# Performance work log

Measured on AMD Instinct MI355X. Metric: run time of the kernel, lower is better.

Reference implementation:

```python
import jax, jax.numpy as jnp
import numpy as np

N_NODES = 50000
N_EDGES = 800000
C_IN = 128
C_OUT = 256
BN_EPS = 1e-5


def setup_inputs() -> dict:
    key = jax.random.key(0)
    k1, k2, k3, k4, k5 = jax.random.split(key, 5)
    x = jax.random.normal(k1, (N_NODES, C_IN), dtype=jnp.float32)
    src = jax.random.randint(k2, (N_EDGES,), 0, N_NODES, dtype=jnp.int64)
    dst = jax.random.randint(k3, (N_EDGES,), 0, N_NODES, dtype=jnp.int64)
    theta_w = jax.random.normal(k4, (C_OUT, C_IN), dtype=jnp.float32) * 0.05
    phi_w = jax.random.normal(k5, (C_OUT, C_IN), dtype=jnp.float32) * 0.05
    gamma = jnp.ones((C_OUT,), dtype=jnp.float32)
    beta = jnp.zeros((C_OUT,), dtype=jnp.float32)
    return {"x": x, "src": src, "dst": dst, "theta_w": theta_w,
            "phi_w": phi_w, "gamma": gamma, "beta": beta}


def reference(x, src, dst, theta_w, phi_w, gamma, beta):
    # gather endpoint features: xi = x[src], xj = x[dst]
    xi = x[src]                      # [E, c_in]
    xj = x[dst]                      # [E, c_in]
    # e_ij = relu(theta(xj - xi) + phi(xi))  -> [E, c_out]
    e = jax.nn.relu((xj - xi) @ theta_w.T + xi @ phi_w.T)
    # scatter-max aggregate per source node; empty segments -> 0 (matches
    # torch.scatter_reduce amax with include_self=False leaving zeros)
    n = x.shape[0]
    agg = jax.ops.segment_max(e, src, num_segments=n)  # [N, c_out]
    agg = jnp.where(jnp.isneginf(agg), jnp.zeros((), agg.dtype), agg)
    # BatchNorm1d (training mode: batch statistics, biased variance)
    mean = jnp.mean(agg, axis=0)
    var = jnp.var(agg, axis=0)
    y = (agg - mean) * jax.lax.rsqrt(var + BN_EPS) * gamma + beta
    return jax.nn.relu(y)
```

## Files before the change

### kernel.cpp

```cpp
#include <hip/hip_runtime.h>

#define N_NODES 50000
#define N_EDGES 800000
#define C_IN 128
#define C_OUT 256
#define BN_EPS 1e-5f
#define NBLK ((N_NODES + 255) / 256)
#define SL 8
#define SLC 32
#define NPB 128
#define PAD 8
#define ECAP 3072

#define HB 782
#define GBX ((N_NODES + 127) / 128)
#define GB (GBX * 4)

using short8  = __attribute__((ext_vector_type(8))) short;
using floatx4 = __attribute__((ext_vector_type(4))) float;
using h2      = __attribute__((ext_vector_type(2))) _Float16;

union UH2 { unsigned int u; h2 h; };
union HS  { _Float16 f; unsigned short s; };

__device__ __forceinline__ h2 pkmax(h2 a, h2 b) {
    return __builtin_elementwise_max(a, b);
}

__device__ __forceinline__ unsigned short f2bf(float f) {
    unsigned int u = __float_as_uint(f);
    u = (u + 0x7fffu + ((u >> 16) & 1u)) >> 16;
    return (unsigned short)u;
}

#define XQ (N_NODES * C_IN / 4)
#define WQ (512 * C_IN / 4)

__global__ __launch_bounds__(256) void prep(
    const float* __restrict__ x, const float* __restrict__ theta,
    const float* __restrict__ phi, const int* __restrict__ src,
    unsigned short* __restrict__ xb, unsigned short* __restrict__ wb,
    int* __restrict__ deg, int* __restrict__ rank)
{
    const int tid = threadIdx.x;
    if (blockIdx.x < HB) {
        const int base = blockIdx.x * 1024 + tid;
        #pragma unroll
        for (int k = 0; k < 4; ++k) {
            int e = base + k * 256;
            if (e < N_EDGES) rank[e] = atomicAdd(&deg[src[e]], 1);
        }
        return;
    }
    int i = (blockIdx.x - HB) * 256 + tid;
    if (i < XQ) {
        float4 vv = ((const float4*)x)[i];
        ((ushort4*)xb)[i] = make_ushort4(f2bf(vv.x), f2bf(vv.y),
                                         f2bf(vv.z), f2bf(vv.w));
    } else if (i < XQ + WQ) {
        int j = i - XQ;
        float4 t;
        if (j < 256 * C_IN / 4) {
            t = ((const float4*)theta)[j];
        } else {
            int k = j - 256 * C_IN / 4;
            float4 th = ((const float4*)theta)[k];
            float4 ph = ((const float4*)phi)[k];
            t = make_float4(ph.x - th.x, ph.y - th.y, ph.z - th.z, ph.w - th.w);
        }
        ((ushort4*)wb)[j] = make_ushort4(f2bf(t.x), f2bf(t.y),
                                         f2bf(t.z), f2bf(t.w));
    }
}

__global__ __launch_bounds__(256) void scan_part(
    const int* __restrict__ deg, int* __restrict__ partials)
{
    __shared__ int s[256];
    const int tid = threadIdx.x;
    int i = blockIdx.x * 256 + tid;
    s[tid] = (i < N_NODES) ? deg[i] : 0;
    __syncthreads();
    for (int d = 128; d > 0; d >>= 1) {
        if (tid < d) s[tid] += s[tid + d];
        __syncthreads();
    }
    if (tid == 0) partials[blockIdx.x] = s[0];
}

__global__ __launch_bounds__(256) void scan_fin(
    const int* __restrict__ deg, const int* __restrict__ partials,
    int* __restrict__ off)
{
    __shared__ int s[256];
    const int tid = threadIdx.x;

    int pv = (tid < NBLK) ? partials[tid] : 0;
    s[tid] = pv;
    __syncthreads();
    for (int d = 1; d < 256; d <<= 1) {
        int t = (tid >= d) ? s[tid - d] : 0;
        __syncthreads();
        s[tid] += t;
        __syncthreads();
    }
    const int blockPrefix = (blockIdx.x == 0) ? 0 : s[blockIdx.x - 1];
    const int total = s[NBLK - 1];
    __syncthreads();

    int i = blockIdx.x * 256 + tid;
    int v = (i < N_NODES) ? deg[i] : 0;
    s[tid] = v;
    __syncthreads();
    for (int d = 1; d < 256; d <<= 1) {
        int t = (tid >= d) ? s[tid - d] : 0;
        __syncthreads();
        s[tid] += t;
        __syncthreads();
    }
    int ex = s[tid] - v + blockPrefix;
    if (i < N_NODES) off[i] = ex;
    if (blockIdx.x == 0 && tid == 0) off[N_NODES] = total;
}

__global__ __launch_bounds__(256) void gemm_scatter(
    const unsigned short* __restrict__ xb,
    const unsigned short* __restrict__ wb,
    unsigned short* __restrict__ u,
    unsigned short* __restrict__ v,
    const int* __restrict__ src, const int* __restrict__ dst,
    const int* __restrict__ off, const int* __restrict__ rank,
    int* __restrict__ edst)
{
    __shared__ unsigned short Bs[128][C_IN + PAD];
    const int tid = threadIdx.x;

    if (blockIdx.x < HB) {
        const int base = blockIdx.x * 1024 + tid;
        #pragma unroll
        for (int k = 0; k < 4; ++k) {
            int e = base + k * 256;
            if (e < N_EDGES) {
                int s = src[e];
                edst[off[s] + rank[e]] = dst[e];
            }
        }
        return;
    }

    const int b = blockIdx.x - HB;
    const int bx = b >> 2;
    const int by = b & 3;
    const int wave = tid >> 6;
    const int lane = tid & 63;
    const int l15 = lane & 15;
    const int quad = lane >> 4;

    {
        int r = tid >> 1;
        int cb = (tid & 1) * 64;
        const uint4* sp = (const uint4*)(wb + (size_t)(by * 128 + r) * C_IN + cb);
        #pragma unroll
        for (int i = 0; i < 8; ++i) *(uint4*)&Bs[r][cb + i * 8] = sp[i];
    }

    const int n0 = bx * 128 + wave * 32 + l15;
    const unsigned short* arow0 = xb + (size_t)min(n0,      N_NODES - 1) * C_IN + quad * 8;
    const unsigned short* arow1 = xb + (size_t)min(n0 + 16, N_NODES - 1) * C_IN + quad * 8;

    __syncthreads();

    floatx4 acc[2][8];
    #pragma unroll
    for (int mi = 0; mi < 2; ++mi)
        #pragma unroll
        for (int ni = 0; ni < 8; ++ni)
            acc[mi][ni] = (floatx4){0.f, 0.f, 0.f, 0.f};

    #pragma unroll
    for (int ks = 0; ks < 4; ++ks) {
        short8 a[2], bfr[8];
        a[0] = *(const short8*)(arow0 + ks * 32);
        a[1] = *(const short8*)(arow1 + ks * 32);
        #pragma unroll
        for (int ni = 0; ni < 8; ++ni)
            bfr[ni] = *(const short8*)&Bs[ni * 16 + l15][ks * 32 + quad * 8];
        #pragma unroll
        for (int mi = 0; mi < 2; ++mi)
            #pragma unroll
            for (int ni = 0; ni < 8; ++ni)
                acc[mi][ni] = __builtin_amdgcn_mfma_f32_16x16x32_bf16(
                    a[mi], bfr[ni], acc[mi][ni], 0, 0, 0);
    }

    const bool is_u = (by < 2);
    #pragma unroll
    for (int mi = 0; mi < 2; ++mi) {
        #pragma unroll
        for (int r = 0; r < 4; ++r) {
            int n = bx * 128 + wave * 32 + mi * 16 + quad * 4 + r;
            if (n >= N_NODES) continue;
            #pragma unroll
            for (int ni = 0; ni < 8; ++ni) {
                int c = by * 128 + ni * 16 + l15;
                HS hv; hv.f = (_Float16)acc[mi][ni][r];
                if (is_u) {
                    int s = c >> 5, o = c & 31;
                    u[((size_t)s * N_NODES + n) * SLC + o] = hv.s;
                } else {
                    int c2 = c - C_OUT;
                    int s = c2 >> 5, o = c2 & 31;
                    v[((size_t)s * N_NODES + n) * SLC + o] = hv.s;
                }
            }
        }
    }
}

__global__ __launch_bounds__(256) void gather_slice(
    const int* __restrict__ off, const int* __restrict__ edst,
    const unsigned short* __restrict__ u, const unsigned short* __restrict__ v,
    float* __restrict__ out, float* __restrict__ sums, float* __restrict__ sumsq)
{
    __shared__ int elds[ECAP];
    __shared__ int offs[NPB + 1];
    __shared__ float red[16][16][4];

    const int slice = blockIdx.x & 7;
    const int chunk = blockIdx.x >> 3;
    const int tid = threadIdx.x;
    const int g16 = tid >> 4;
    const int l16 = tid & 15;
    const int es  = l16 >> 2;
    const int c4  = l16 & 3;
    const int c16 = c4 * 16;
    const int cp  = c4 * 8 + es * 2;

    const int cn   = chunk * NPB;
    const int nend = min(cn + NPB, N_NODES);
    const int nloc = nend - cn;

    const int s0  = off[cn];
    const int cnt = off[nend] - s0;
    for (int t = tid; t <= nloc; t += 256) offs[t] = off[cn + t];
    const bool fits = (cnt <= ECAP);
    if (fits)
        for (int t = tid; t < cnt; t += 256) elds[t] = edst[s0 + t];
    __syncthreads();

    const char* ub = (const char*)(u + (size_t)slice * N_NODES * SLC);
    const unsigned short* vb = v + (size_t)slice * N_NODES * SLC;

    float s1_0 = 0.f, s1_1 = 0.f, s2_0 = 0.f, s2_1 = 0.f;

    auto gather_all = [&](auto fetch) {
        #pragma unroll 1
        for (int i = 0; i < NPB / 16; ++i) {
            const int nl = i * 16 + g16;
            const int n = cn + nl;
            if (n >= N_NODES) continue;
            const int start = offs[nl];
            const int end   = offs[nl + 1];

            UH2 m0, m1, m2, m3;
            m0.u = m1.u = m2.u = m3.u = 0xFC00FC00u;

            const int nit = (end - start + 15) >> 4;
            const int lim = end - 1;
            int b16 = start + es;
            for (int r = 0; r < nit; ++r, b16 += 16) {
                int i0 = min(b16,      lim);
                int i1 = min(b16 + 4,  lim);
                int i2 = min(b16 + 8,  lim);
                int i3 = min(b16 + 12, lim);
                int d0 = fetch(i0);
                int d1 = fetch(i1);
                int d2 = fetch(i2);
                int d3 = fetch(i3);
                uint4 w0 = *(const uint4*)(ub + ((d0 << 6) | c16));
                uint4 w1 = *(const uint4*)(ub + ((d1 << 6) | c16));
                uint4 w2 = *(const uint4*)(ub + ((d2 << 6) | c16));
                uint4 w3 = *(const uint4*)(ub + ((d3 << 6) | c16));
                UH2 a_, b_, c_, e_;
                a_.u = w0.x; b_.u = w1.x; c_.u = w2.x; e_.u = w3.x;
                m0.h = pkmax(m0.h, pkmax(pkmax(a_.h, b_.h), pkmax(c_.h, e_.h)));
                a_.u = w0.y; b_.u = w1.y; c_.u = w2.y; e_.u = w3.y;
                m1.h = pkmax(m1.h, pkmax(pkmax(a_.h, b_.h), pkmax(c_.h, e_.h)));
                a_.u = w0.z; b_.u = w1.z; c_.u = w2.z; e_.u = w3.z;
                m2.h = pkmax(m2.h, pkmax(pkmax(a_.h, b_.h), pkmax(c_.h, e_.h)));
                a_.u = w0.w; b_.u = w1.w; c_.u = w2.w; e_.u = w3.w;
                m3.h = pkmax(m3.h, pkmax(pkmax(a_.h, b_.h), pkmax(c_.h, e_.h)));
            }

            UH2 t;
            t.u = (unsigned)__shfl_xor((int)m0.u, 4); m0.h = pkmax(m0.h, t.h);
            t.u = (unsigned)__shfl_xor((int)m1.u, 4); m1.h = pkmax(m1.h, t.h);
            t.u = (unsigned)__shfl_xor((int)m2.u, 4); m2.h = pkmax(m2.h, t.h);
            t.u = (unsigned)__shfl_xor((int)m3.u, 4); m3.h = pkmax(m3.h, t.h);
            t.u = (unsigned)__shfl_xor((int)m0.u, 8); m0.h = pkmax(m0.h, t.h);
            t.u = (unsigned)__shfl_xor((int)m1.u, 8); m1.h = pkmax(m1.h, t.h);
            t.u = (unsigned)__shfl_xor((int)m2.u, 8); m2.h = pkmax(m2.h, t.h);
            t.u = (unsigned)__shfl_xor((int)m3.u, 8); m3.h = pkmax(m3.h, t.h);

            UH2 s01, s23, mm;
            s01.u = (es & 1) ? m1.u : m0.u;
            s23.u = (es & 1) ? m3.u : m2.u;
            mm.u  = (es & 2) ? s23.u : s01.u;

            UH2 wv; wv.u = *(const unsigned int*)(vb + (size_t)n * SLC + cp);
            float a0 = fmaxf((float)wv.h[0] + (float)mm.h[0], 0.f);
            float a1 = fmaxf((float)wv.h[1] + (float)mm.h[1], 0.f);

            *(float2*)(out + (size_t)n * C_OUT + slice * SLC + cp) =
                make_float2(a0, a1);
            s1_0 += a0; s1_1 += a1;
            s2_0 += a0 * a0; s2_1 += a1 * a1;
        }
    };

    if (fits) gather_all([&](int i) { return elds[i - s0]; });
    else      gather_all([&](int i) { return edst[i]; });

    __syncthreads();
    red[g16][l16][0] = s1_0; red[g16][l16][1] = s1_1;
    red[g16][l16][2] = s2_0; red[g16][l16][3] = s2_1;
    __syncthreads();
    if (tid < 16) {
        const int tt = tid;
        float r0 = 0.f, r1 = 0.f, r2 = 0.f, r3 = 0.f;
        #pragma unroll
        for (int g = 0; g < 16; ++g) {
            r0 += red[g][tt][0]; r1 += red[g][tt][1];
            r2 += red[g][tt][2]; r3 += red[g][tt][3];
        }
        const int c = slice * SLC + ((tt & 3) * 8 + (tt >> 2) * 2);
        atomicAdd(&sums[c + 0], r0);
        atomicAdd(&sums[c + 1], r1);
        atomicAdd(&sumsq[c + 0], r2);
        atomicAdd(&sumsq[c + 1], r3);
    }
}

__global__ __launch_bounds__(256) void bn_apply(
    float* __restrict__ out, const float* __restrict__ sums,
    const float* __restrict__ sumsq, const float* __restrict__ gamma,
    const float* __restrict__ beta)
{
    __shared__ float cA[C_OUT], cB[C_OUT];
    const int tid = threadIdx.x;
    {
        const float inv_n = 1.f / (float)N_NODES;
        const float mean = sums[tid] * inv_n;
        const float var = sumsq[tid] * inv_n - mean * mean;
        const float s = rsqrtf(var + BN_EPS) * gamma[tid];
        cA[tid] = s;
        cB[tid] = beta[tid] - mean * s;
    }
    __syncthreads();

    const int c4 = (tid * 4) & (C_OUT - 1);
    const float4 A = *(const float4*)(cA + c4);
    const float4 B = *(const float4*)(cB + c4);
    const int base = blockIdx.x * 1024 + tid;
    #pragma unroll
    for (int k = 0; k < 4; ++k) {
        const int i = base + k * 256;
        float4 o = ((float4*)out)[i];
        o.x = fmaxf(o.x * A.x + B.x, 0.f);
        o.y = fmaxf(o.y * A.y + B.y, 0.f);
        o.z = fmaxf(o.z * A.z + B.z, 0.f);
        o.w = fmaxf(o.w * A.w + B.w, 0.f);
        ((float4*)out)[i] = o;
    }
}

extern "C" void kernel_launch(void* const* d_in, const int* in_sizes, int n_in,
                              void* d_out, int out_size, void* d_ws, size_t ws_size,
                              hipStream_t stream) {
    const float* x     = (const float*)d_in[0];
    const int*   src   = (const int*)d_in[1];
    const int*   dst   = (const int*)d_in[2];
    const float* theta = (const float*)d_in[3];
    const float* phi   = (const float*)d_in[4];
    const float* gamma = (const float*)d_in[5];
    const float* beta  = (const float*)d_in[6];
    float* out = (float*)d_out;

    char* ws = (char*)d_ws;
    const size_t uv_elems = (size_t)N_NODES * C_OUT;
    unsigned short* u = (unsigned short*)ws;
    unsigned short* v = u + uv_elems;
    float* sums   = (float*)(v + uv_elems);
    float* sumsq  = sums + C_OUT;
    int*   deg    = (int*)(sumsq + C_OUT);
    int*   off    = deg + N_NODES;
    int*   rank   = off + N_NODES + 4;
    int*   edst   = rank + N_EDGES;
    int*   partials = edst + N_EDGES;
    unsigned short* xb = (unsigned short*)(partials + NBLK + 8);
    unsigned short* wb = xb + (size_t)N_NODES * C_IN;

    hipMemsetAsync(sums, 0, (2 * C_OUT + N_NODES) * sizeof(int), stream);

    prep<<<HB + (XQ + WQ + 255) / 256, 256, 0, stream>>>(
        x, theta, phi, src, xb, wb, deg, rank);

    scan_part<<<NBLK, 256, 0, stream>>>(deg, partials);
    scan_fin<<<NBLK, 256, 0, stream>>>(deg, partials, off);

    gemm_scatter<<<HB + GB, 256, 0, stream>>>(
        xb, wb, u, v, src, dst, off, rank, edst);

    const int chunks = (N_NODES + NPB - 1) / NPB;
    gather_slice<<<chunks * SL, 256, 0, stream>>>(
        off, edst, u, v, out, sums, sumsq);

    bn_apply<<<(N_NODES * C_OUT / 4) / 1024, 256, 0, stream>>>(
        out, sums, sumsq, gamma, beta);
}
```

Before: 234.4 us.

## Store aggregate as fp16 in place of v and narrow edge indices to 16-bit

```diff
diff --git a/kernel.cpp b/kernel.cpp
--- a/kernel.cpp
+++ b/kernel.cpp
@@ -40,7 +40,7 @@
     const float* __restrict__ x, const float* __restrict__ theta,
     const float* __restrict__ phi, const int* __restrict__ src,
     unsigned short* __restrict__ xb, unsigned short* __restrict__ wb,
-    int* __restrict__ deg, int* __restrict__ rank)
+    int* __restrict__ deg, unsigned short* __restrict__ rank)
 {
     const int tid = threadIdx.x;
     if (blockIdx.x < HB) {
@@ -48,7 +48,8 @@
         #pragma unroll
         for (int k = 0; k < 4; ++k) {
             int e = base + k * 256;
-            if (e < N_EDGES) rank[e] = atomicAdd(&deg[src[e]], 1);
+            if (e < N_EDGES)
+                rank[e] = (unsigned short)atomicAdd(&deg[src[e]], 1);
         }
         return;
     }
@@ -129,8 +130,8 @@
     unsigned short* __restrict__ u,
     unsigned short* __restrict__ v,
     const int* __restrict__ src, const int* __restrict__ dst,
-    const int* __restrict__ off, const int* __restrict__ rank,
-    int* __restrict__ edst)
+    const int* __restrict__ off, const unsigned short* __restrict__ rank,
+    unsigned short* __restrict__ edst)
 {
     __shared__ unsigned short Bs[128][C_IN + PAD];
     const int tid = threadIdx.x;
@@ -142,7 +143,7 @@
             int e = base + k * 256;
             if (e < N_EDGES) {
                 int s = src[e];
-                edst[off[s] + rank[e]] = dst[e];
+                edst[off[s] + (int)rank[e]] = (unsigned short)dst[e];
             }
         }
         return;
@@ -218,11 +219,11 @@
 }
 
 __global__ __launch_bounds__(256) void gather_slice(
-    const int* __restrict__ off, const int* __restrict__ edst,
-    const unsigned short* __restrict__ u, const unsigned short* __restrict__ v,
-    float* __restrict__ out, float* __restrict__ sums, float* __restrict__ sumsq)
-{
-    __shared__ int elds[ECAP];
+    const int* __restrict__ off, const unsigned short* __restrict__ edst,
+    const unsigned short* __restrict__ u, unsigned short* __restrict__ v,
+    float* __restrict__ sums, float* __restrict__ sumsq)
+{
+    __shared__ unsigned short elds[ECAP];
     __shared__ int offs[NPB + 1];
     __shared__ float red[16][16][4];
 
@@ -249,7 +250,7 @@
     __syncthreads();
 
     const char* ub = (const char*)(u + (size_t)slice * N_NODES * SLC);
-    const unsigned short* vb = v + (size_t)slice * N_NODES * SLC;
+    unsigned short* vb = v + (size_t)slice * N_NODES * SLC;
 
     float s1_0 = 0.f, s1_1 = 0.f, s2_0 = 0.f, s2_1 = 0.f;
 
@@ -307,19 +308,23 @@
             s23.u = (es & 1) ? m3.u : m2.u;
             mm.u  = (es & 2) ? s23.u : s01.u;
 
-            UH2 wv; wv.u = *(const unsigned int*)(vb + (size_t)n * SLC + cp);
+            unsigned int* vp = (unsigned int*)(vb + (size_t)n * SLC + cp);
+            UH2 wv; wv.u = *vp;
             float a0 = fmaxf((float)wv.h[0] + (float)mm.h[0], 0.f);
             float a1 = fmaxf((float)wv.h[1] + (float)mm.h[1], 0.f);
 
-            *(float2*)(out + (size_t)n * C_OUT + slice * SLC + cp) =
-                make_float2(a0, a1);
+            UH2 pw;
+            pw.h[0] = (_Float16)a0;
+            pw.h[1] = (_Float16)a1;
+            *vp = pw.u;
+
             s1_0 += a0; s1_1 += a1;
             s2_0 += a0 * a0; s2_1 += a1 * a1;
         }
     };
 
-    if (fits) gather_all([&](int i) { return elds[i - s0]; });
-    else      gather_all([&](int i) { return edst[i]; });
+    if (fits) gather_all([&](int i) { return (int)elds[i - s0]; });
+    else      gather_all([&](int i) { return (int)edst[i]; });
 
     __syncthreads();
     red[g16][l16][0] = s1_0; red[g16][l16][1] = s1_1;
@@ -342,6 +347,7 @@
 }
 
 __global__ __launch_bounds__(256) void bn_apply(
+    const unsigned short* __restrict__ agg,
     float* __restrict__ out, const float* __restrict__ sums,
     const float* __restrict__ sumsq, const float* __restrict__ gamma,
     const float* __restrict__ beta)
@@ -358,20 +364,36 @@
     }
     __syncthreads();
 
-    const int c4 = (tid * 4) & (C_OUT - 1);
-    const float4 A = *(const float4*)(cA + c4);
-    const float4 B = *(const float4*)(cB + c4);
-    const int base = blockIdx.x * 1024 + tid;
-    #pragma unroll
-    for (int k = 0; k < 4; ++k) {
-        const int i = base + k * 256;
-        float4 o = ((float4*)out)[i];
-        o.x = fmaxf(o.x * A.x + B.x, 0.f);
-        o.y = fmaxf(o.y * A.y + B.y, 0.f);
-        o.z = fmaxf(o.z * A.z + B.z, 0.f);
-        o.w = fmaxf(o.w * A.w + B.w, 0.f);
-        ((float4*)out)[i] = o;
-    }
+    const size_t base = (size_t)blockIdx.x * 2048 + (size_t)tid * 8;
+    const int slice  = (int)(base / ((size_t)N_NODES * SLC));
+    const int within = (int)(base % ((size_t)N_NODES * SLC));
+    const int n  = within >> 5;
+    const int c  = slice * SLC + (within & 31);
+
+    uint4 w = *(const uint4*)(agg + base);
+    const float4 A0 = *(const float4*)(cA + c);
+    const float4 A1 = *(const float4*)(cA + c + 4);
+    const float4 B0 = *(const float4*)(cB + c);
+    const float4 B1 = *(const float4*)(cB + c + 4);
+
+    UH2 t;
+    float4 o0, o1;
+    t.u = w.x;
+    o0.x = fmaxf((float)t.h[0] * A0.x + B0.x, 0.f);
+    o0.y = fmaxf((float)t.h[1] * A0.y + B0.y, 0.f);
+    t.u = w.y;
+    o0.z = fmaxf((float)t.h[0] * A0.z + B0.z, 0.f);
+    o0.w = fmaxf((float)t.h[1] * A0.w + B0.w, 0.f);
+    t.u = w.z;
+    o1.x = fmaxf((float)t.h[0] * A1.x + B1.x, 0.f);
+    o1.y = fmaxf((float)t.h[1] * A1.y + B1.y, 0.f);
+    t.u = w.w;
+    o1.z = fmaxf((float)t.h[0] * A1.z + B1.z, 0.f);
+    o1.w = fmaxf((float)t.h[1] * A1.w + B1.w, 0.f);
+
+    float* op = out + (size_t)n * C_OUT + c;
+    *(float4*)op = o0;
+    *(float4*)(op + 4) = o1;
 }
 
 extern "C" void kernel_launch(void* const* d_in, const int* in_sizes, int n_in,
@@ -394,9 +416,9 @@
     float* sumsq  = sums + C_OUT;
     int*   deg    = (int*)(sumsq + C_OUT);
     int*   off    = deg + N_NODES;
-    int*   rank   = off + N_NODES + 4;
-    int*   edst   = rank + N_EDGES;
-    int*   partials = edst + N_EDGES;
+    unsigned short* rank = (unsigned short*)(off + N_NODES + 4);
+    unsigned short* edst = rank + N_EDGES;
+    int*   partials = (int*)(edst + N_EDGES);
     unsigned short* xb = (unsigned short*)(partials + NBLK + 8);
     unsigned short* wb = xb + (size_t)N_NODES * C_IN;
 
@@ -413,8 +435,8 @@
 
     const int chunks = (N_NODES + NPB - 1) / NPB;
     gather_slice<<<chunks * SL, 256, 0, stream>>>(
-        off, edst, u, v, out, sums, sumsq);
-
-    bn_apply<<<(N_NODES * C_OUT / 4) / 1024, 256, 0, stream>>>(
-        out, sums, sumsq, gamma, beta);
-}
+        off, edst, u, v, sums, sumsq);
+
+    bn_apply<<<(int)(((size_t)N_NODES * C_OUT) / 2048), 256, 0, stream>>>(
+        v, out, sums, sumsq, gamma, beta);
+}
```

Result: faster. 229.2 us (-2.2%).
